# Kernel tuning notes

Hardware: AMD Instinct MI355X
Metric: run time of the kernel (lower is better)

Reference implementation:

```python
import jax, jax.numpy as jnp
import numpy as np

N = 100000   # nodes
E = 1600000  # edges
IN = 512     # in_channels
H = 256      # hidden_channels
C = 40       # out_channels
BITS = 8     # INT8 fake quantization


def fake_quant(x, bits=BITS):
    """Symmetric per-tensor quantize-dequantize with straight-through estimator."""
    qmax = float(2 ** (bits - 1) - 1)
    scale = jnp.max(jnp.abs(x)) / qmax + 1e-12
    q = jnp.clip(jnp.round(x / scale), -qmax - 1.0, qmax) * scale
    # STE: forward = q, backward = identity
    return x + jax.lax.stop_gradient(q - x)


def quant_linear(x, w, b):
    # LinearQuantized: fake-quant inputs and weights, fp accumulate
    return fake_quant(x) @ fake_quant(w).T + b


def gcn_propagate(x, edge_index):
    """Symmetric-normalized sparse propagation: out = D^-1/2 A D^-1/2 x."""
    src, dst = edge_index[0], edge_index[1]
    deg = jax.ops.segment_sum(jnp.ones((E,), x.dtype), dst, num_segments=N)
    dinv = jnp.where(deg > 0, jax.lax.rsqrt(jnp.maximum(deg, 1.0)), 0.0)
    coef = dinv[src] * dinv[dst]                     # [E]
    msgs = x[src] * coef[:, None]                    # [E, C]
    return jax.ops.segment_sum(msgs, dst, num_segments=N)  # [N, C]


def setup_inputs() -> dict:
    key = jax.random.key(0)
    ks = jax.random.split(key, 6)
    x = jax.random.normal(ks[0], (N, IN), jnp.float32)
    edge_index = jax.random.randint(ks[1], (2, E), 0, N, dtype=jnp.int32)
    w1 = jax.random.normal(ks[2], (H, IN), jnp.float32) * (1.0 / np.sqrt(IN))
    b1 = jnp.zeros((H,), jnp.float32)
    w2 = jax.random.normal(ks[3], (C, H), jnp.float32) * (1.0 / np.sqrt(H))
    b2 = jnp.zeros((C,), jnp.float32)
    return {"x": x, "edge_index": edge_index, "w1": w1, "b1": b1, "w2": w2, "b2": b2}


def reference(x, edge_index, w1, b1, w2, b2):
    # dropout: identity in eval mode
    h = jax.nn.relu(quant_linear(x, w1, b1))         # [N, H]
    z = quant_linear(h, w2, b2)                      # [N, C]
    z = gcn_propagate(z, edge_index)                 # [N, C]
    return jax.nn.log_softmax(z, axis=1)
```

## Files before the change

### kernel.cpp

```cpp
#include <hip/hip_runtime.h>
#include <hip/hip_bf16.h>
#include <stdint.h>
#include <stddef.h>

#define NN   100000
#define NE   1600000
#define INC  512
#define HID  256
#define OC   40
#define OCP  48

#define LDS1 144
#define LDSB2 272

#define NBKT ((NN + 255) / 256)
#define NMT1 ((NN + 127) / 128)

#define ABS_X_BLKS  2048
#define ABS_W1_BLKS 128
#define ABS_W2_BLKS 16

typedef float  f32x4  __attribute__((ext_vector_type(4)));
typedef int    i32x4  __attribute__((ext_vector_type(4)));

__device__ unsigned g_amax_bits[4];
__device__ float    g_dinv[NN];
__device__ signed char g_qx[(size_t)NN * INC];
__device__ signed char g_qw1[HID * INC];
__device__ signed char g_qw2[OCP * HID];
__device__ float    g_h[(size_t)NN * HID];
__device__ float    g_z[(size_t)NN * OC];
__device__ unsigned g_chist[NBKT];
__device__ unsigned g_cstart[NBKT + 1];
__device__ unsigned g_ccur[NBKT];
__device__ uint2    g_bin[NE];
__device__ unsigned g_rowstart[NN + 1];
__device__ int      g_csr_src[NE];

__device__ __forceinline__ float quantf(float v, float rs) {
    return fminf(fmaxf(rintf(v * rs), -128.0f), 127.0f);
}
__device__ __forceinline__ int pack4(float a, float b, float c, float d, float rs) {
    int q0 = (int)quantf(a, rs), q1 = (int)quantf(b, rs);
    int q2 = (int)quantf(c, rs), q3 = (int)quantf(d, rs);
    return (q0 & 255) | ((q1 & 255) << 8) | ((q2 & 255) << 16) | ((q3 & 255) << 24);
}

__global__ void init_kernel() {
    int idx = blockIdx.x * blockDim.x + threadIdx.x;
    int stride = gridDim.x * blockDim.x;
    for (int i = idx; i < NBKT; i += stride) g_chist[i] = 0u;
    for (int i = idx; i < (OCP * HID) / 4; i += stride) ((int*)g_qw2)[i] = 0;
    if (idx < 4) g_amax_bits[idx] = 0u;
}

__global__ void chist_kernel(const int* __restrict__ ei) {
    const int* dst = ei + NE;
    __shared__ unsigned hist[NBKT];
    int t = threadIdx.x;
    for (int i = t; i < NBKT; i += 256) hist[i] = 0u;
    __syncthreads();
    int idx = blockIdx.x * 256 + t;
    int stride = gridDim.x * 256;
    for (int e = idx; e < NE; e += stride) atomicAdd(&hist[dst[e] >> 8], 1u);
    __syncthreads();
    for (int i = t; i < NBKT; i += 256) {
        unsigned c = hist[i];
        if (c) atomicAdd(&g_chist[i], c);
    }
}

__global__ void cscan_kernel() {
    int t = threadIdx.x;
    unsigned v = (t < NBKT) ? g_chist[t] : 0u;
    int lane = t & 63, wv = t >> 6;
    unsigned sc = v;
#pragma unroll
    for (int off = 1; off < 64; off <<= 1) {
        unsigned n = __shfl_up(sc, off, 64);
        if (lane >= off) sc += n;
    }
    __shared__ unsigned ws[8];
    if (lane == 63) ws[wv] = sc;
    __syncthreads();
    unsigned woff = 0;
    for (int w = 0; w < 8; w++) if (w < wv) woff += ws[w];
    unsigned excl = woff + sc - v;
    if (t < NBKT) { g_cstart[t] = excl; g_ccur[t] = excl; }
    if (t == 0) g_cstart[NBKT] = NE;
}

#define BIN_BLOCKS 400
#define BIN_EPB    (NE / BIN_BLOCKS)
__global__ void bin_kernel(const int* __restrict__ ei) {
    const int* srcp = ei;
    const int* dstp = ei + NE;
    __shared__ unsigned hist[NBKT];
    __shared__ unsigned base[NBKT];
    int t = threadIdx.x;
    int e0 = blockIdx.x * BIN_EPB, e1 = e0 + BIN_EPB;
    for (int i = t; i < NBKT; i += 256) hist[i] = 0u;
    __syncthreads();
    for (int e = e0 + t; e < e1; e += 256) atomicAdd(&hist[dstp[e] >> 8], 1u);
    __syncthreads();
    for (int i = t; i < NBKT; i += 256) {
        unsigned c = hist[i];
        base[i] = c ? atomicAdd(&g_ccur[i], c) : 0u;
        hist[i] = 0u;
    }
    __syncthreads();
    for (int e = e0 + t; e < e1; e += 256) {
        int d = dstp[e], s = srcp[e];
        int b = d >> 8;
        unsigned r = atomicAdd(&hist[b], 1u);
        g_bin[base[b] + r] = make_uint2((unsigned)s, (unsigned)d);
    }
}

__global__ void local_kernel() {
    int b = blockIdx.x, t = threadIdx.x;
    unsigned e0 = g_cstart[b], e1 = g_cstart[b + 1];
    __shared__ unsigned hist[256];
    __shared__ unsigned curs[256];
    __shared__ unsigned wsum[4];
    hist[t] = 0u;
    __syncthreads();
    for (unsigned e = e0 + t; e < e1; e += 256) atomicAdd(&hist[g_bin[e].y & 255], 1u);
    __syncthreads();
    unsigned v = hist[t];
    int lane = t & 63, wv = t >> 6;
    unsigned sc = v;
#pragma unroll
    for (int off = 1; off < 64; off <<= 1) {
        unsigned n = __shfl_up(sc, off, 64);
        if (lane >= off) sc += n;
    }
    if (lane == 63) wsum[wv] = sc;
    __syncthreads();
    unsigned woff = 0;
    for (int w = 0; w < 4; w++) if (w < wv) woff += wsum[w];
    unsigned excl = woff + sc - v;
    int node = b * 256 + t;
    if (node < NN) {
        g_rowstart[node] = e0 + excl;
        g_dinv[node] = v ? rsqrtf((float)v) : 0.0f;
    }
    if (b == 0 && t == 0) g_rowstart[NN] = NE;
    curs[t] = excl;
    __syncthreads();
    for (unsigned e = e0 + t; e < e1; e += 256) {
        uint2 ed = g_bin[e];
        unsigned r = atomicAdd(&curs[ed.y & 255], 1u);
        g_csr_src[e0 + r] = (int)ed.x;
    }
}

__global__ void absmax3_kernel(const float* __restrict__ x,
                               const float* __restrict__ w1,
                               const float* __restrict__ w2) {
    const float* src; int n4, slot, bbase, nb;
    int b = blockIdx.x;
    if (b < ABS_X_BLKS) {
        src = x;  n4 = (NN * INC) / 4;  slot = 0; bbase = 0;                       nb = ABS_X_BLKS;
    } else if (b < ABS_X_BLKS + ABS_W1_BLKS) {
        src = w1; n4 = (HID * INC) / 4; slot = 1; bbase = ABS_X_BLKS;              nb = ABS_W1_BLKS;
    } else {
        src = w2; n4 = (OC * HID) / 4;  slot = 2; bbase = ABS_X_BLKS + ABS_W1_BLKS; nb = ABS_W2_BLKS;
    }
    int idx = (b - bbase) * blockDim.x + threadIdx.x;
    int stride = nb * blockDim.x;
    const f32x4* s4 = (const f32x4*)src;
    float m = 0.0f;
    for (int i = idx; i < n4; i += stride) {
        f32x4 v = s4[i];
        m = fmaxf(m, fmaxf(fmaxf(fabsf(v.x), fabsf(v.y)),
                           fmaxf(fabsf(v.z), fabsf(v.w))));
    }
#pragma unroll
    for (int off = 32; off > 0; off >>= 1) m = fmaxf(m, __shfl_xor(m, off, 64));
    __shared__ float sm[4];
    if ((threadIdx.x & 63) == 0) sm[threadIdx.x >> 6] = m;
    __syncthreads();
    if (threadIdx.x == 0) {
        float mm = fmaxf(fmaxf(sm[0], sm[1]), fmaxf(sm[2], sm[3]));
        atomicMax(&g_amax_bits[slot], __float_as_uint(mm));
    }
}

__global__ void quantx_kernel(const float* __restrict__ src, int n16) {
    float rs = 1.0f / (__uint_as_float(g_amax_bits[0]) / 127.0f + 1e-12f);
    int idx = blockIdx.x * blockDim.x + threadIdx.x;
    int stride = gridDim.x * blockDim.x;
    i32x4* d = (i32x4*)g_qx;
    for (int i = idx; i < n16; i += stride) {
        const f32x4* s = (const f32x4*)(src + (size_t)i * 16);
        f32x4 v0 = s[0], v1 = s[1], v2 = s[2], v3 = s[3];
        i32x4 o;
        o[0] = pack4(v0.x, v0.y, v0.z, v0.w, rs);
        o[1] = pack4(v1.x, v1.y, v1.z, v1.w, rs);
        o[2] = pack4(v2.x, v2.y, v2.z, v2.w, rs);
        o[3] = pack4(v3.x, v3.y, v3.z, v3.w, rs);
        d[i] = o;
    }
}

__global__ void quantw_kernel(const float* __restrict__ w1, const float* __restrict__ w2) {
    const float* src; int* dst; int nint, slot, bbase, nb;
    int b = blockIdx.x;
    if (b < 128) { src = w1; dst = (int*)g_qw1; nint = (HID * INC) / 4; slot = 1; bbase = 0;   nb = 128; }
    else         { src = w2; dst = (int*)g_qw2; nint = (OC * HID) / 4;  slot = 2; bbase = 128; nb = 16;  }
    float rs = 1.0f / (__uint_as_float(g_amax_bits[slot]) / 127.0f + 1e-12f);
    int idx = (b - bbase) * blockDim.x + threadIdx.x;
    int stride = nb * blockDim.x;
    for (int i = idx; i < nint; i += stride) {
        f32x4 v = *(const f32x4*)(src + (size_t)i * 4);
        dst[i] = pack4(v.x, v.y, v.z, v.w, rs);
    }
}

__launch_bounds__(256)
__global__ void gemm1_kernel(const float* __restrict__ b1) {
    __shared__ char lA[2][128 * LDS1];
    __shared__ char lB[2][128 * LDS1];
    int group = blockIdx.x >> 4;
    int ntile = (blockIdx.x >> 3) & 1;
    int mtile = group * 8 + (blockIdx.x & 7);
    if (mtile >= NMT1) return;
    int t = threadIdx.x;
    int lane = t & 63, wv = t >> 6;
    int quad = lane >> 4, l16 = lane & 15;
    int mq = wv >> 1, nq = wv & 1;

    int srow = t >> 3;
    int sch  = t & 7;

    const signed char* xb[4];
    const signed char* wb[4];
#pragma unroll
    for (int p = 0; p < 4; p++) {
        int gr = mtile * 128 + p * 32 + srow; if (gr >= NN) gr = NN - 1;
        xb[p] = g_qx + (size_t)gr * INC + sch * 16;
        wb[p] = g_qw1 + (size_t)(ntile * 128 + p * 32 + srow) * INC + sch * 16;
    }

    i32x4 av[4], bv[4];
#pragma unroll
    for (int p = 0; p < 4; p++) {
        av[p] = *(const i32x4*)(xb[p]);
        bv[p] = *(const i32x4*)(wb[p]);
    }

    i32x4 acc[4][4] = {};
#pragma unroll 1
    for (int kit = 0; kit < 4; kit++) {
        int bs = kit & 1;
#pragma unroll
        for (int p = 0; p < 4; p++) {
            int row = p * 32 + srow;
            *(i32x4*)(lA[bs] + row * LDS1 + sch * 16) = av[p];
            *(i32x4*)(lB[bs] + row * LDS1 + sch * 16) = bv[p];
        }
        if (kit + 1 < 4) {
#pragma unroll
            for (int p = 0; p < 4; p++) {
                av[p] = *(const i32x4*)(xb[p] + (kit + 1) * 128);
                bv[p] = *(const i32x4*)(wb[p] + (kit + 1) * 128);
            }
        }
        __syncthreads();
#pragma unroll
        for (int ks = 0; ks < 2; ks++) {
            int cs = ks * 64 + quad * 16;
            i32x4 a[4], b[4];
#pragma unroll
            for (int i = 0; i < 4; i++)
                a[i] = *(const i32x4*)(lA[bs] + (mq * 64 + i * 16 + l16) * LDS1 + cs);
#pragma unroll
            for (int j = 0; j < 4; j++)
                b[j] = *(const i32x4*)(lB[bs] + (nq * 64 + j * 16 + l16) * LDS1 + cs);
#pragma unroll
            for (int i = 0; i < 4; i++)
#pragma unroll
                for (int j = 0; j < 4; j++)
                    acc[i][j] = __builtin_amdgcn_mfma_i32_16x16x64_i8(a[i], b[j], acc[i][j], 0, 0, 0);
        }
    }
    float s = (__uint_as_float(g_amax_bits[0]) / 127.0f + 1e-12f)
            * (__uint_as_float(g_amax_bits[1]) / 127.0f + 1e-12f);
    float lmax = 0.0f;
#pragma unroll
    for (int j = 0; j < 4; j++) {
        int col = ntile * 128 + nq * 64 + j * 16 + l16;
        float bias = b1[col];
#pragma unroll
        for (int i = 0; i < 4; i++) {
#pragma unroll
            for (int r = 0; r < 4; r++) {
                int grow = mtile * 128 + mq * 64 + i * 16 + quad * 4 + r;
                float v = fmaxf(s * (float)acc[i][j][r] + bias, 0.0f);
                lmax = fmaxf(lmax, v);
                if (grow < NN) g_h[(size_t)grow * HID + col] = v;
            }
        }
    }
#pragma unroll
    for (int off = 32; off > 0; off >>= 1) lmax = fmaxf(lmax, __shfl_xor(lmax, off, 64));
    if (lane == 0) atomicMax(&g_amax_bits[3], __float_as_uint(lmax));
}

__launch_bounds__(256)
__global__ void gemm2_kernel(const float* __restrict__ b2) {
    __shared__ char lB2[OCP * LDSB2];
    __shared__ char lA2[128 * LDS1];
    int t = threadIdx.x;
    int mtile = blockIdx.x;
    int lane = t & 63, wv = t >> 6;
    int quad = lane >> 4, l16 = lane & 15;

#pragma unroll
    for (int p = 0; p < 3; p++) {
        int ci = p * 256 + t;
        int row = ci >> 4, ch = ci & 15;
        *(i32x4*)(lB2 + row * LDSB2 + ch * 16) =
            *(const i32x4*)(g_qw2 + row * 256 + ch * 16);
    }

    float scale_h = __uint_as_float(g_amax_bits[3]) / 127.0f + 1e-12f;
    float rs = 1.0f / scale_h;
    int srow = t >> 3, sch = t & 7;
    const float* hbase[4];
#pragma unroll
    for (int p = 0; p < 4; p++) {
        int gr = mtile * 128 + p * 32 + srow; if (gr >= NN) gr = NN - 1;
        hbase[p] = g_h + (size_t)gr * HID + sch * 16;
    }

    i32x4 acc[2][3] = {};
#pragma unroll 1
    for (int kit = 0; kit < 2; kit++) {
        if (kit) __syncthreads();
#pragma unroll
        for (int p = 0; p < 4; p++) {
            int row = p * 32 + srow;
            const float* hp = hbase[p] + kit * 128;
            f32x4 v0 = *(const f32x4*)(hp);
            f32x4 v1 = *(const f32x4*)(hp + 4);
            f32x4 v2 = *(const f32x4*)(hp + 8);
            f32x4 v3 = *(const f32x4*)(hp + 12);
            i32x4 o;
            o[0] = pack4(v0.x, v0.y, v0.z, v0.w, rs);
            o[1] = pack4(v1.x, v1.y, v1.z, v1.w, rs);
            o[2] = pack4(v2.x, v2.y, v2.z, v2.w, rs);
            o[3] = pack4(v3.x, v3.y, v3.z, v3.w, rs);
            *(i32x4*)(lA2 + row * LDS1 + sch * 16) = o;
        }
        __syncthreads();
#pragma unroll
        for (int ks = 0; ks < 2; ks++) {
            int cs = ks * 64 + quad * 16;
            i32x4 a[2], b[3];
#pragma unroll
            for (int i = 0; i < 2; i++)
                a[i] = *(const i32x4*)(lA2 + (wv * 32 + i * 16 + l16) * LDS1 + cs);
#pragma unroll
            for (int j = 0; j < 3; j++)
                b[j] = *(const i32x4*)(lB2 + (j * 16 + l16) * LDSB2 + kit * 128 + cs);
#pragma unroll
            for (int i = 0; i < 2; i++)
#pragma unroll
                for (int j = 0; j < 3; j++)
                    acc[i][j] = __builtin_amdgcn_mfma_i32_16x16x64_i8(a[i], b[j], acc[i][j], 0, 0, 0);
        }
    }
    float s = scale_h * (__uint_as_float(g_amax_bits[2]) / 127.0f + 1e-12f);
#pragma unroll
    for (int j = 0; j < 3; j++) {
        int col = j * 16 + l16;
        float bias = (col < OC) ? b2[col] : 0.0f;
#pragma unroll
        for (int i = 0; i < 2; i++) {
#pragma unroll
            for (int r = 0; r < 4; r++) {
                int grow = mtile * 128 + wv * 32 + i * 16 + quad * 4 + r;
                if (col < OC && grow < NN)
                    g_z[(size_t)grow * OC + col] = s * (float)acc[i][j][r] + bias;
            }
        }
    }
}

__launch_bounds__(256)
__global__ void gather_kernel(float* __restrict__ out) {
    int node = (blockIdx.x * 256 + threadIdx.x) >> 6;
    int lane = threadIdx.x & 63;
    if (node >= NN) return;
    unsigned e0 = g_rowstart[node], e1 = g_rowstart[node + 1];
    float dinvd = g_dinv[node];
    bool ch = (lane < OC);
    float acc0 = 0.0f, acc1 = 0.0f;
    unsigned e = e0;
    for (; e + 8 <= e1; e += 8) {
        int s0 = g_csr_src[e],     s1 = g_csr_src[e + 1];
        int s2 = g_csr_src[e + 2], s3 = g_csr_src[e + 3];
        int s4 = g_csr_src[e + 4], s5 = g_csr_src[e + 5];
        int s6 = g_csr_src[e + 6], s7 = g_csr_src[e + 7];
        float c0 = g_dinv[s0], c1 = g_dinv[s1], c2 = g_dinv[s2], c3 = g_dinv[s3];
        float c4 = g_dinv[s4], c5 = g_dinv[s5], c6 = g_dinv[s6], c7 = g_dinv[s7];
        float z0 = ch ? g_z[(size_t)s0 * OC + lane] : 0.0f;
        float z1 = ch ? g_z[(size_t)s1 * OC + lane] : 0.0f;
        float z2 = ch ? g_z[(size_t)s2 * OC + lane] : 0.0f;
        float z3 = ch ? g_z[(size_t)s3 * OC + lane] : 0.0f;
        float z4 = ch ? g_z[(size_t)s4 * OC + lane] : 0.0f;
        float z5 = ch ? g_z[(size_t)s5 * OC + lane] : 0.0f;
        float z6 = ch ? g_z[(size_t)s6 * OC + lane] : 0.0f;
        float z7 = ch ? g_z[(size_t)s7 * OC + lane] : 0.0f;
        acc0 += (z0 * c0 + z1 * c1) + (z2 * c2 + z3 * c3);
        acc1 += (z4 * c4 + z5 * c5) + (z6 * c6 + z7 * c7);
    }
    for (; e + 4 <= e1; e += 4) {
        int s0 = g_csr_src[e],     s1 = g_csr_src[e + 1];
        int s2 = g_csr_src[e + 2], s3 = g_csr_src[e + 3];
        float c0 = g_dinv[s0], c1 = g_dinv[s1], c2 = g_dinv[s2], c3 = g_dinv[s3];
        float z0 = ch ? g_z[(size_t)s0 * OC + lane] : 0.0f;
        float z1 = ch ? g_z[(size_t)s1 * OC + lane] : 0.0f;
        float z2 = ch ? g_z[(size_t)s2 * OC + lane] : 0.0f;
        float z3 = ch ? g_z[(size_t)s3 * OC + lane] : 0.0f;
        acc0 += (z0 * c0 + z1 * c1) + (z2 * c2 + z3 * c3);
    }
    for (; e < e1; e++) {
        int s0 = g_csr_src[e];
        float z0 = ch ? g_z[(size_t)s0 * OC + lane] : 0.0f;
        acc1 += z0 * g_dinv[s0];
    }
    float acc = (acc0 + acc1) * dinvd;
    float m = ch ? acc : -1e30f;
#pragma unroll
    for (int off = 32; off > 0; off >>= 1) m = fmaxf(m, __shfl_xor(m, off, 64));
    float ex = ch ? __expf(acc - m) : 0.0f;
    float ssum = ex;
#pragma unroll
    for (int off = 32; off > 0; off >>= 1) ssum += __shfl_xor(ssum, off, 64);
    float lg = __logf(ssum);
    if (ch) out[(size_t)node * OC + lane] = acc - m - lg;
}

extern "C" void kernel_launch(void* const* d_in, const int* in_sizes, int n_in,
                              void* d_out, int out_size, void* d_ws, size_t ws_size,
                              hipStream_t stream) {
    const float* x  = (const float*)d_in[0];
    const int*   ei = (const int*)d_in[1];
    const float* w1 = (const float*)d_in[2];
    const float* b1 = (const float*)d_in[3];
    const float* w2 = (const float*)d_in[4];
    const float* b2 = (const float*)d_in[5];
    float* out = (float*)d_out;
    (void)d_ws; (void)ws_size; (void)in_sizes; (void)n_in; (void)out_size;

    init_kernel<<<1024, 256, 0, stream>>>();
    chist_kernel<<<256, 256, 0, stream>>>(ei);
    cscan_kernel<<<1, 512, 0, stream>>>();
    bin_kernel<<<BIN_BLOCKS, 256, 0, stream>>>(ei);
    local_kernel<<<NBKT, 256, 0, stream>>>();
    absmax3_kernel<<<ABS_X_BLKS + ABS_W1_BLKS + ABS_W2_BLKS, 256, 0, stream>>>(x, w1, w2);
    quantx_kernel<<<3200, 256, 0, stream>>>(x, (NN * INC) / 16);
    quantw_kernel<<<144, 256, 0, stream>>>(w1, w2);
    gemm1_kernel<<<((NMT1 + 7) / 8) * 16, 256, 0, stream>>>(b1);
    gemm2_kernel<<<(NN + 127) / 128, 256, 0, stream>>>(b2);
    gather_kernel<<<(NN + 3) / 4, 256, 0, stream>>>(out);
}
```

Before: 586.3 us.

## Merge independent graph-build and quantization stages into shared kernel launches

The separate absmax, histogram, bin, local-sort, quantize and GEMM1 launches are combined into fewer launches. Each merged kernel dispatches independent work by block index (absmax with chist, quant with bin, gemm1 with local CSR build). The aim is to cut launch gaps and let the small graph-preprocessing work overlap with bandwidth-heavy quantization and the GEMM. The costs are heavier shared-memory and register footprints for the combined kernels, and the CSR blocks in gemm1 scheduling after the GEMM tiles, which may tail.

```diff
diff --git a/kernel.cpp b/kernel.cpp
--- a/kernel.cpp
+++ b/kernel.cpp
@@ -15,10 +15,21 @@
 
 #define NBKT ((NN + 255) / 256)
 #define NMT1 ((NN + 127) / 128)
+#define GEMM1_BLKS (((NMT1 + 7) / 8) * 16)
 
 #define ABS_X_BLKS  2048
 #define ABS_W1_BLKS 128
 #define ABS_W2_BLKS 16
+#define ABS_TOT     (ABS_X_BLKS + ABS_W1_BLKS + ABS_W2_BLKS)
+#define CHIST_BLKS  256
+#define QX_BLKS     3200
+#define QW1_BLKS    128
+#define QW2_BLKS    16
+#define BIN_BLOCKS  400
+#define BIN_EPB     (NE / BIN_BLOCKS)
+#define L3_QW1_BASE QX_BLKS
+#define L3_QW2_BASE (QX_BLKS + QW1_BLKS)
+#define L3_BIN_BASE (QX_BLKS + QW1_BLKS + QW2_BLKS)
 
 typedef float  f32x4  __attribute__((ext_vector_type(4)));
 typedef int    i32x4  __attribute__((ext_vector_type(4)));
@@ -54,19 +65,52 @@
     if (idx < 4) g_amax_bits[idx] = 0u;
 }
 
-__global__ void chist_kernel(const int* __restrict__ ei) {
-    const int* dst = ei + NE;
-    __shared__ unsigned hist[NBKT];
+__global__ void __launch_bounds__(256) absmax_chist_kernel(const float* __restrict__ x,
+                                                           const float* __restrict__ w1,
+                                                           const float* __restrict__ w2,
+                                                           const int* __restrict__ ei) {
+    __shared__ unsigned shist[NBKT];
+    __shared__ float sm[4];
+    int b = blockIdx.x;
     int t = threadIdx.x;
-    for (int i = t; i < NBKT; i += 256) hist[i] = 0u;
-    __syncthreads();
-    int idx = blockIdx.x * 256 + t;
-    int stride = gridDim.x * 256;
-    for (int e = idx; e < NE; e += stride) atomicAdd(&hist[dst[e] >> 8], 1u);
-    __syncthreads();
-    for (int i = t; i < NBKT; i += 256) {
-        unsigned c = hist[i];
-        if (c) atomicAdd(&g_chist[i], c);
+    if (b < ABS_TOT) {
+        const float* src; int n4, slot, bbase, nb;
+        if (b < ABS_X_BLKS) {
+            src = x;  n4 = (NN * INC) / 4;  slot = 0; bbase = 0;                       nb = ABS_X_BLKS;
+        } else if (b < ABS_X_BLKS + ABS_W1_BLKS) {
+            src = w1; n4 = (HID * INC) / 4; slot = 1; bbase = ABS_X_BLKS;              nb = ABS_W1_BLKS;
+        } else {
+            src = w2; n4 = (OC * HID) / 4;  slot = 2; bbase = ABS_X_BLKS + ABS_W1_BLKS; nb = ABS_W2_BLKS;
+        }
+        int idx = (b - bbase) * 256 + t;
+        int stride = nb * 256;
+        const f32x4* s4 = (const f32x4*)src;
+        float m = 0.0f;
+        for (int i = idx; i < n4; i += stride) {
+            f32x4 v = s4[i];
+            m = fmaxf(m, fmaxf(fmaxf(fabsf(v.x), fabsf(v.y)),
+                               fmaxf(fabsf(v.z), fabsf(v.w))));
+        }
+#pragma unroll
+        for (int off = 32; off > 0; off >>= 1) m = fmaxf(m, __shfl_xor(m, off, 64));
+        if ((t & 63) == 0) sm[t >> 6] = m;
+        __syncthreads();
+        if (t == 0) {
+            float mm = fmaxf(fmaxf(sm[0], sm[1]), fmaxf(sm[2], sm[3]));
+            atomicMax(&g_amax_bits[slot], __float_as_uint(mm));
+        }
+    } else {
+        const int* dst = ei + NE;
+        for (int i = t; i < NBKT; i += 256) shist[i] = 0u;
+        __syncthreads();
+        int idx = (b - ABS_TOT) * 256 + t;
+        int stride = CHIST_BLKS * 256;
+        for (int e = idx; e < NE; e += stride) atomicAdd(&shist[dst[e] >> 8], 1u);
+        __syncthreads();
+        for (int i = t; i < NBKT; i += 256) {
+            unsigned c = shist[i];
+            if (c) atomicAdd(&g_chist[i], c);
+        }
     }
 }
 
@@ -90,143 +134,111 @@
     if (t == 0) g_cstart[NBKT] = NE;
 }
 
-#define BIN_BLOCKS 400
-#define BIN_EPB    (NE / BIN_BLOCKS)
-__global__ void bin_kernel(const int* __restrict__ ei) {
-    const int* srcp = ei;
-    const int* dstp = ei + NE;
+__global__ void __launch_bounds__(256) quant_bin_kernel(const float* __restrict__ x,
+                                                        const float* __restrict__ w1,
+                                                        const float* __restrict__ w2,
+                                                        const int* __restrict__ ei) {
     __shared__ unsigned hist[NBKT];
     __shared__ unsigned base[NBKT];
+    int b = blockIdx.x;
     int t = threadIdx.x;
-    int e0 = blockIdx.x * BIN_EPB, e1 = e0 + BIN_EPB;
-    for (int i = t; i < NBKT; i += 256) hist[i] = 0u;
-    __syncthreads();
-    for (int e = e0 + t; e < e1; e += 256) atomicAdd(&hist[dstp[e] >> 8], 1u);
-    __syncthreads();
-    for (int i = t; i < NBKT; i += 256) {
-        unsigned c = hist[i];
-        base[i] = c ? atomicAdd(&g_ccur[i], c) : 0u;
-        hist[i] = 0u;
-    }
-    __syncthreads();
-    for (int e = e0 + t; e < e1; e += 256) {
-        int d = dstp[e], s = srcp[e];
-        int b = d >> 8;
-        unsigned r = atomicAdd(&hist[b], 1u);
-        g_bin[base[b] + r] = make_uint2((unsigned)s, (unsigned)d);
-    }
-}
-
-__global__ void local_kernel() {
-    int b = blockIdx.x, t = threadIdx.x;
-    unsigned e0 = g_cstart[b], e1 = g_cstart[b + 1];
-    __shared__ unsigned hist[256];
-    __shared__ unsigned curs[256];
-    __shared__ unsigned wsum[4];
-    hist[t] = 0u;
-    __syncthreads();
-    for (unsigned e = e0 + t; e < e1; e += 256) atomicAdd(&hist[g_bin[e].y & 255], 1u);
-    __syncthreads();
-    unsigned v = hist[t];
-    int lane = t & 63, wv = t >> 6;
-    unsigned sc = v;
-#pragma unroll
-    for (int off = 1; off < 64; off <<= 1) {
-        unsigned n = __shfl_up(sc, off, 64);
-        if (lane >= off) sc += n;
-    }
-    if (lane == 63) wsum[wv] = sc;
-    __syncthreads();
-    unsigned woff = 0;
-    for (int w = 0; w < 4; w++) if (w < wv) woff += wsum[w];
-    unsigned excl = woff + sc - v;
-    int node = b * 256 + t;
-    if (node < NN) {
-        g_rowstart[node] = e0 + excl;
-        g_dinv[node] = v ? rsqrtf((float)v) : 0.0f;
-    }
-    if (b == 0 && t == 0) g_rowstart[NN] = NE;
-    curs[t] = excl;
-    __syncthreads();
-    for (unsigned e = e0 + t; e < e1; e += 256) {
-        uint2 ed = g_bin[e];
-        unsigned r = atomicAdd(&curs[ed.y & 255], 1u);
-        g_csr_src[e0 + r] = (int)ed.x;
-    }
-}
-
-__global__ void absmax3_kernel(const float* __restrict__ x,
-                               const float* __restrict__ w1,
-                               const float* __restrict__ w2) {
-    const float* src; int n4, slot, bbase, nb;
-    int b = blockIdx.x;
-    if (b < ABS_X_BLKS) {
-        src = x;  n4 = (NN * INC) / 4;  slot = 0; bbase = 0;                       nb = ABS_X_BLKS;
-    } else if (b < ABS_X_BLKS + ABS_W1_BLKS) {
-        src = w1; n4 = (HID * INC) / 4; slot = 1; bbase = ABS_X_BLKS;              nb = ABS_W1_BLKS;
+    if (b < QX_BLKS) {
+        float rs = 1.0f / (__uint_as_float(g_amax_bits[0]) / 127.0f + 1e-12f);
+        int idx = b * 256 + t;
+        int stride = QX_BLKS * 256;
+        int n16 = (NN * INC) / 16;
+        i32x4* d = (i32x4*)g_qx;
+        for (int i = idx; i < n16; i += stride) {
+            const f32x4* s = (const f32x4*)(x + (size_t)i * 16);
+            f32x4 v0 = s[0], v1 = s[1], v2 = s[2], v3 = s[3];
+            i32x4 o;
+            o[0] = pack4(v0.x, v0.y, v0.z, v0.w, rs);
+            o[1] = pack4(v1.x, v1.y, v1.z, v1.w, rs);
+            o[2] = pack4(v2.x, v2.y, v2.z, v2.w, rs);
+            o[3] = pack4(v3.x, v3.y, v3.z, v3.w, rs);
+            d[i] = o;
+        }
+    } else if (b < L3_BIN_BASE) {
+        const float* src; int* dst; int nint, slot, bbase, nb;
+        if (b < L3_QW2_BASE) { src = w1; dst = (int*)g_qw1; nint = (HID * INC) / 4; slot = 1; bbase = L3_QW1_BASE; nb = QW1_BLKS; }
+        else                 { src = w2; dst = (int*)g_qw2; nint = (OC * HID) / 4;  slot = 2; bbase = L3_QW2_BASE; nb = QW2_BLKS; }
+        float rs = 1.0f / (__uint_as_float(g_amax_bits[slot]) / 127.0f + 1e-12f);
+        int idx = (b - bbase) * 256 + t;
+        int stride = nb * 256;
+        for (int i = idx; i < nint; i += stride) {
+            f32x4 v = *(const f32x4*)(src + (size_t)i * 4);
+            dst[i] = pack4(v.x, v.y, v.z, v.w, rs);
+        }
     } else {
-        src = w2; n4 = (OC * HID) / 4;  slot = 2; bbase = ABS_X_BLKS + ABS_W1_BLKS; nb = ABS_W2_BLKS;
-    }
-    int idx = (b - bbase) * blockDim.x + threadIdx.x;
-    int stride = nb * blockDim.x;
-    const f32x4* s4 = (const f32x4*)src;
-    float m = 0.0f;
-    for (int i = idx; i < n4; i += stride) {
-        f32x4 v = s4[i];
-        m = fmaxf(m, fmaxf(fmaxf(fabsf(v.x), fabsf(v.y)),
-                           fmaxf(fabsf(v.z), fabsf(v.w))));
-    }
-#pragma unroll
-    for (int off = 32; off > 0; off >>= 1) m = fmaxf(m, __shfl_xor(m, off, 64));
-    __shared__ float sm[4];
-    if ((threadIdx.x & 63) == 0) sm[threadIdx.x >> 6] = m;
-    __syncthreads();
-    if (threadIdx.x == 0) {
-        float mm = fmaxf(fmaxf(sm[0], sm[1]), fmaxf(sm[2], sm[3]));
-        atomicMax(&g_amax_bits[slot], __float_as_uint(mm));
-    }
-}
-
-__global__ void quantx_kernel(const float* __restrict__ src, int n16) {
-    float rs = 1.0f / (__uint_as_float(g_amax_bits[0]) / 127.0f + 1e-12f);
-    int idx = blockIdx.x * blockDim.x + threadIdx.x;
-    int stride = gridDim.x * blockDim.x;
-    i32x4* d = (i32x4*)g_qx;
-    for (int i = idx; i < n16; i += stride) {
-        const f32x4* s = (const f32x4*)(src + (size_t)i * 16);
-        f32x4 v0 = s[0], v1 = s[1], v2 = s[2], v3 = s[3];
-        i32x4 o;
-        o[0] = pack4(v0.x, v0.y, v0.z, v0.w, rs);
-        o[1] = pack4(v1.x, v1.y, v1.z, v1.w, rs);
-        o[2] = pack4(v2.x, v2.y, v2.z, v2.w, rs);
-        o[3] = pack4(v3.x, v3.y, v3.z, v3.w, rs);
-        d[i] = o;
-    }
-}
-
-__global__ void quantw_kernel(const float* __restrict__ w1, const float* __restrict__ w2) {
-    const float* src; int* dst; int nint, slot, bbase, nb;
-    int b = blockIdx.x;
-    if (b < 128) { src = w1; dst = (int*)g_qw1; nint = (HID * INC) / 4; slot = 1; bbase = 0;   nb = 128; }
-    else         { src = w2; dst = (int*)g_qw2; nint = (OC * HID) / 4;  slot = 2; bbase = 128; nb = 16;  }
-    float rs = 1.0f / (__uint_as_float(g_amax_bits[slot]) / 127.0f + 1e-12f);
-    int idx = (b - bbase) * blockDim.x + threadIdx.x;
-    int stride = nb * blockDim.x;
-    for (int i = idx; i < nint; i += stride) {
-        f32x4 v = *(const f32x4*)(src + (size_t)i * 4);
-        dst[i] = pack4(v.x, v.y, v.z, v.w, rs);
-    }
-}
-
-__launch_bounds__(256)
-__global__ void gemm1_kernel(const float* __restrict__ b1) {
+        const int* srcp = ei;
+        const int* dstp = ei + NE;
+        int bb = b - L3_BIN_BASE;
+        int e0 = bb * BIN_EPB, e1 = e0 + BIN_EPB;
+        for (int i = t; i < NBKT; i += 256) hist[i] = 0u;
+        __syncthreads();
+        for (int e = e0 + t; e < e1; e += 256) atomicAdd(&hist[dstp[e] >> 8], 1u);
+        __syncthreads();
+        for (int i = t; i < NBKT; i += 256) {
+            unsigned c = hist[i];
+            base[i] = c ? atomicAdd(&g_ccur[i], c) : 0u;
+            hist[i] = 0u;
+        }
+        __syncthreads();
+        for (int e = e0 + t; e < e1; e += 256) {
+            int d = dstp[e], s = srcp[e];
+            int bk = d >> 8;
+            unsigned r = atomicAdd(&hist[bk], 1u);
+            g_bin[base[bk] + r] = make_uint2((unsigned)s, (unsigned)d);
+        }
+    }
+}
+
+__global__ void __launch_bounds__(256) gemm1_local_kernel(const float* __restrict__ b1) {
     __shared__ char lA[2][128 * LDS1];
     __shared__ char lB[2][128 * LDS1];
+    int t = threadIdx.x;
+    if (blockIdx.x >= GEMM1_BLKS) {
+        int b = blockIdx.x - GEMM1_BLKS;
+        unsigned* hist = (unsigned*)lA;
+        unsigned* curs = hist + 256;
+        unsigned* wsum = curs + 256;
+        unsigned e0 = g_cstart[b], e1 = g_cstart[b + 1];
+        hist[t] = 0u;
+        __syncthreads();
+        for (unsigned e = e0 + t; e < e1; e += 256) atomicAdd(&hist[g_bin[e].y & 255], 1u);
+        __syncthreads();
+        unsigned v = hist[t];
+        int lane = t & 63, wv = t >> 6;
+        unsigned sc = v;
+#pragma unroll
+        for (int off = 1; off < 64; off <<= 1) {
+            unsigned n = __shfl_up(sc, off, 64);
+            if (lane >= off) sc += n;
+        }
+        if (lane == 63) wsum[wv] = sc;
+        __syncthreads();
+        unsigned woff = 0;
+        for (int w = 0; w < 4; w++) if (w < wv) woff += wsum[w];
+        unsigned excl = woff + sc - v;
+        int node = b * 256 + t;
+        if (node < NN) {
+            g_rowstart[node] = e0 + excl;
+            g_dinv[node] = v ? rsqrtf((float)v) : 0.0f;
+        }
+        if (b == 0 && t == 0) g_rowstart[NN] = NE;
+        curs[t] = excl;
+        __syncthreads();
+        for (unsigned e = e0 + t; e < e1; e += 256) {
+            uint2 ed = g_bin[e];
+            unsigned r = atomicAdd(&curs[ed.y & 255], 1u);
+            g_csr_src[e0 + r] = (int)ed.x;
+        }
+        return;
+    }
     int group = blockIdx.x >> 4;
     int ntile = (blockIdx.x >> 3) & 1;
     int mtile = group * 8 + (blockIdx.x & 7);
     if (mtile >= NMT1) return;
-    int t = threadIdx.x;
     int lane = t & 63, wv = t >> 6;
     int quad = lane >> 4, l16 = lane & 15;
     int mq = wv >> 1, nq = wv & 1;
@@ -456,15 +468,11 @@
     float* out = (float*)d_out;
     (void)d_ws; (void)ws_size; (void)in_sizes; (void)n_in; (void)out_size;
 
-    init_kernel<<<1024, 256, 0, stream>>>();
-    chist_kernel<<<256, 256, 0, stream>>>(ei);
+    init_kernel<<<64, 256, 0, stream>>>();
+    absmax_chist_kernel<<<ABS_TOT + CHIST_BLKS, 256, 0, stream>>>(x, w1, w2, ei);
     cscan_kernel<<<1, 512, 0, stream>>>();
-    bin_kernel<<<BIN_BLOCKS, 256, 0, stream>>>(ei);
-    local_kernel<<<NBKT, 256, 0, stream>>>();
-    absmax3_kernel<<<ABS_X_BLKS + ABS_W1_BLKS + ABS_W2_BLKS, 256, 0, stream>>>(x, w1, w2);
-    quantx_kernel<<<3200, 256, 0, stream>>>(x, (NN * INC) / 16);
-    quantw_kernel<<<144, 256, 0, stream>>>(w1, w2);
-    gemm1_kernel<<<((NMT1 + 7) / 8) * 16, 256, 0, stream>>>(b1);
+    quant_bin_kernel<<<L3_BIN_BASE + BIN_BLOCKS, 256, 0, stream>>>(x, w1, w2, ei);
+    gemm1_local_kernel<<<GEMM1_BLKS + NBKT, 256, 0, stream>>>(b1);
     gemm2_kernel<<<(NN + 127) / 128, 256, 0, stream>>>(b2);
     gather_kernel<<<(NN + 3) / 4, 256, 0, stream>>>(out);
 }
```

New measurement: 567.3 us. -3.2%, faster.
